# Kernel optimization log

Measured on AMD Instinct MI355X. Metric: run time of the kernel, lower is better.

The kernel has to match this reference:

```python
import jax, jax.numpy as jnp
import numpy as np

DIM = 1024
HEADS = 16
DIM_HEAD = 64
INNER = HEADS * DIM_HEAD  # 1024
P = INNER  # num_param_tokens
B, N = 4, 2048
LN_EPS = 1e-5
NORM_EPS = 1e-12


def _pattention(x, key_tok, val_tok):
    # x: [..., dim_in]; key_tok: [P, dim_in]; val_tok: [P, dim_out]
    scale = key_tok.shape[1] ** (-0.5)
    sim = jnp.einsum('bnd,pd->bnp', x, key_tok) * scale
    # F.normalize(p=2, dim=-1) with eps=1e-12
    nrm = jnp.maximum(jnp.linalg.norm(sim, axis=-1, keepdims=True), NORM_EPS)
    attn = jax.nn.gelu(sim / nrm, approximate=False)  # torch F.gelu default = exact erf
    return jnp.einsum('bnp,pe->bne', attn, val_tok)


def setup_inputs() -> dict:
    key = jax.random.key(0)
    ks = jax.random.split(key, 11)
    d = {
        'x': jax.random.normal(ks[0], (B, N, DIM), dtype=jnp.float32),
        'ln_gamma': jnp.ones((DIM,), dtype=jnp.float32),
        'ln_beta': jnp.zeros((DIM,), dtype=jnp.float32),
        'q_key': jax.random.normal(ks[1], (P, DIM), dtype=jnp.float32),
        'q_val': jax.random.normal(ks[2], (P, INNER), dtype=jnp.float32),
        'k_key': jax.random.normal(ks[3], (P, DIM), dtype=jnp.float32),
        'k_val': jax.random.normal(ks[4], (P, INNER), dtype=jnp.float32),
        'v_key': jax.random.normal(ks[5], (P, DIM), dtype=jnp.float32),
        'v_val': jax.random.normal(ks[6], (P, INNER), dtype=jnp.float32),
        'o_key': jax.random.normal(ks[7], (P, INNER), dtype=jnp.float32),
        'o_val': jax.random.normal(ks[8], (P, DIM), dtype=jnp.float32),
    }
    return d


def reference(x, ln_gamma, ln_beta, q_key, q_val, k_key, k_val, v_key, v_val, o_key, o_val):
    # LayerNorm (torch default: elementwise affine, eps=1e-5)
    mu = jnp.mean(x, axis=-1, keepdims=True)
    var = jnp.mean(jnp.square(x - mu), axis=-1, keepdims=True)
    x_norm = (x - mu) / jnp.sqrt(var + LN_EPS) * ln_gamma + ln_beta

    q = _pattention(x_norm, q_key, q_val)  # [B, N, INNER]
    k = _pattention(x_norm, k_key, k_val)
    v = _pattention(x_norm, v_key, v_val)

    # b n (h d) -> b h n d
    def split_heads(t):
        return t.reshape(B, N, HEADS, DIM_HEAD).transpose(0, 2, 1, 3)

    q, k, v = split_heads(q), split_heads(k), split_heads(v)
    scale = DIM_HEAD ** (-0.5)
    dots = jnp.einsum('bhnd,bhmd->bhnm', q, k) * scale  # [B, H, N, N]
    attn = jax.nn.softmax(dots, axis=-1)  # dropout p=0 -> identity
    out = jnp.einsum('bhnm,bhmd->bhnd', attn, v)
    out = out.transpose(0, 2, 1, 3).reshape(B, N, INNER)  # b h n d -> b n (h d)
    return _pattention(out, o_key, o_val)
```

## Files before the change

kernel.cpp:

```cpp
#include <hip/hip_runtime.h>
#include <hip/hip_bf16.h>
#include <stdint.h>

#define DIMSZ 1024
#define BN_TOT 8192
#define NSEQ 2048
#define NHEADS 16
#define DHEAD 64

typedef __attribute__((ext_vector_type(8))) __bf16 bf16x8;
typedef __attribute__((ext_vector_type(4))) float f32x4;

__device__ __forceinline__ float bf2f(ushort u) {
  return __uint_as_float(((uint32_t)u) << 16);
}
__device__ __forceinline__ ushort f2bf(float f) {
  uint32_t u = __float_as_uint(f);
  u += 0x7FFFu + ((u >> 16) & 1u);
  return (ushort)(u >> 16);
}
__device__ __forceinline__ uint32_t cvt_pk_bf16(float lo, float hi) {
  uint32_t r;
  asm("v_cvt_pk_bf16_f32 %0, %1, %2" : "=v"(r) : "v"(lo), "v"(hi));
  return r;
}
__device__ __forceinline__ void gl_lds16(const ushort* g, ushort* l) {
  __builtin_amdgcn_global_load_lds(
      (const __attribute__((address_space(1))) void*)g,
      (__attribute__((address_space(3))) void*)l, 16, 0, 0);
}

__global__ __launch_bounds__(256) void layernorm_k(
    const float* __restrict__ x, const float* __restrict__ gamma,
    const float* __restrict__ beta, ushort* __restrict__ xn) {
  const int row = blockIdx.x;
  const int tid = threadIdx.x;
  const float* xr = x + (size_t)row * DIMSZ;
  float4 v = *(const float4*)(xr + tid * 4);
  float s = v.x + v.y + v.z + v.w;
  float ss = v.x * v.x + v.y * v.y + v.z * v.z + v.w * v.w;
#pragma unroll
  for (int o = 1; o < 64; o <<= 1) { s += __shfl_xor(s, o); ss += __shfl_xor(ss, o); }
  __shared__ float red[2][4];
  const int wid = tid >> 6;
  if ((tid & 63) == 0) { red[0][wid] = s; red[1][wid] = ss; }
  __syncthreads();
  s = red[0][0] + red[0][1] + red[0][2] + red[0][3];
  ss = red[1][0] + red[1][1] + red[1][2] + red[1][3];
  const float mu = s * (1.0f / DIMSZ);
  const float var = ss * (1.0f / DIMSZ) - mu * mu;
  const float rstd = rsqrtf(var + 1e-5f);
  float4 g = *(const float4*)(gamma + tid * 4);
  float4 bb = *(const float4*)(beta + tid * 4);
  ushort4 o4;
  o4.x = f2bf((v.x - mu) * rstd * g.x + bb.x);
  o4.y = f2bf((v.y - mu) * rstd * g.y + bb.y);
  o4.z = f2bf((v.z - mu) * rstd * g.z + bb.z);
  o4.w = f2bf((v.w - mu) * rstd * g.w + bb.w);
  *(ushort4*)(xn + (size_t)row * DIMSZ + tid * 4) = o4;
}

__global__ __launch_bounds__(256) void normgelu_k(
    const float* __restrict__ sim, ushort* __restrict__ out) {
  const int row = blockIdx.x;
  const int tid = threadIdx.x;
  const float* sr = sim + (size_t)row * DIMSZ;
  float4 v = *(const float4*)(sr + tid * 4);
  float ss = v.x * v.x + v.y * v.y + v.z * v.z + v.w * v.w;
#pragma unroll
  for (int o = 1; o < 64; o <<= 1) ss += __shfl_xor(ss, o);
  __shared__ float red[4];
  if ((tid & 63) == 0) red[tid >> 6] = ss;
  __syncthreads();
  ss = red[0] + red[1] + red[2] + red[3];
  const float inv = 1.0f / fmaxf(sqrtf(ss), 1e-12f);
  ushort4 o4;
  float x0;
  x0 = v.x * inv; o4.x = f2bf(0.5f * x0 * (1.0f + erff(x0 * 0.70710678118654752f)));
  x0 = v.y * inv; o4.y = f2bf(0.5f * x0 * (1.0f + erff(x0 * 0.70710678118654752f)));
  x0 = v.z * inv; o4.z = f2bf(0.5f * x0 * (1.0f + erff(x0 * 0.70710678118654752f)));
  x0 = v.w * inv; o4.w = f2bf(0.5f * x0 * (1.0f + erff(x0 * 0.70710678118654752f)));
  *(ushort4*)(out + (size_t)row * DIMSZ + tid * 4) = o4;
}

__global__ void cvt_k(const float* __restrict__ in, ushort* __restrict__ out, int n) {
  int i = (blockIdx.x * 256 + threadIdx.x) * 4;
  if (i < n) {
    float4 v = *(const float4*)(in + i);
    ushort4 o;
    o.x = f2bf(v.x); o.y = f2bf(v.y); o.z = f2bf(v.z); o.w = f2bf(v.w);
    *(ushort4*)(out + i) = o;
  }
}

__global__ __launch_bounds__(256) void transpose_cvt_k(
    const float* __restrict__ in, ushort* __restrict__ out) {
  __shared__ float t[32][33];
  const int tx = threadIdx.x & 31;
  const int ty = threadIdx.x >> 5;
  const int bx = blockIdx.x * 32;
  const int by = blockIdx.y * 32;
#pragma unroll
  for (int i = 0; i < 32; i += 8)
    t[ty + i][tx] = in[(size_t)(by + ty + i) * DIMSZ + bx + tx];
  __syncthreads();
#pragma unroll
  for (int i = 0; i < 32; i += 8)
    out[(size_t)(bx + ty + i) * DIMSZ + by + tx] = f2bf(t[tx][ty + i]);
}

__global__ __launch_bounds__(256) void transpose_v_k(
    const ushort* __restrict__ vb, ushort* __restrict__ vt) {
  __shared__ ushort t[32][33];
  const int bh = blockIdx.x;
  const int nt = blockIdx.y;
  const int dt = blockIdx.z;
  const int b = bh >> 4, h = bh & 15;
  const int tx = threadIdx.x & 31;
  const int ty = threadIdx.x >> 5;
  const size_t inbase = ((size_t)b * NSEQ + nt * 32) * DIMSZ + h * DHEAD + dt * 32;
#pragma unroll
  for (int i = 0; i < 32; i += 8)
    t[ty + i][tx] = vb[inbase + (size_t)(ty + i) * DIMSZ + tx];
  __syncthreads();
  const size_t outbase = ((size_t)bh * DHEAD + dt * 32) * NSEQ + nt * 32;
#pragma unroll
  for (int i = 0; i < 32; i += 8)
    vt[outbase + (size_t)(ty + i) * NSEQ + tx] = t[tx][ty + i];
}

template <int OUT_BF16>
__global__ __launch_bounds__(256) void gemm_nt_k(
    const ushort* __restrict__ A, const ushort* __restrict__ B,
    void* __restrict__ Cout, int M, int N, int K) {
  __shared__ ushort As[3][128 * 32];
  __shared__ ushort Bs[3][128 * 32];
  const int tid = threadIdx.x;
  const int lane = tid & 63;
  const int wid = tid >> 6;
  const int i0 = blockIdx.x * 128;
  const int n0 = blockIdx.y * 128;
  const int wr = (wid >> 1) * 64;
  const int wc = (wid & 1) * 64;
  f32x4 acc[4][4];
#pragma unroll
  for (int m = 0; m < 4; ++m)
#pragma unroll
    for (int n = 0; n < 4; ++n) acc[m][n] = (f32x4){0.f, 0.f, 0.f, 0.f};
  const int fr = lane & 15;
  const int g = lane >> 4;
  const int kg = (g ^ ((fr >> 1) & 3)) * 8;
  const int srow = wid * 32 + (lane >> 2);
  const int skc = ((lane & 3) ^ ((lane >> 3) & 3)) * 8;
  const ushort* Ag = A + (size_t)(i0 + srow) * K + skc;
  const ushort* Bg = B + (size_t)(n0 + srow) * K + skc;
  const int wb = wid * 1024;

#define STAGE_TILE(tt, bb)                                      \
  do {                                                          \
    gl_lds16(Ag + (tt) * 32, &As[bb][wb]);                      \
    gl_lds16(Ag + (size_t)16 * K + (tt) * 32, &As[bb][wb + 512]); \
    gl_lds16(Bg + (tt) * 32, &Bs[bb][wb]);                      \
    gl_lds16(Bg + (size_t)16 * K + (tt) * 32, &Bs[bb][wb + 512]); \
  } while (0)

  const int nt = K >> 5;
  STAGE_TILE(0, 0);
  STAGE_TILE(1, 1);
  asm volatile("s_waitcnt vmcnt(4)" ::: "memory");
  __builtin_amdgcn_s_barrier();

  int cur = 0;
  for (int t = 0; t < nt; ++t) {
    if (t + 2 < nt) {
      const int nb = (cur >= 1) ? cur - 1 : cur + 2;
      STAGE_TILE(t + 2, nb);
    }
    bf16x8 af[4], bfr[4];
#pragma unroll
    for (int m = 0; m < 4; ++m)
      af[m] = *(const bf16x8*)&As[cur][(wr + m * 16 + fr) * 32 + kg];
#pragma unroll
    for (int n = 0; n < 4; ++n)
      bfr[n] = *(const bf16x8*)&Bs[cur][(wc + n * 16 + fr) * 32 + kg];
#pragma unroll
    for (int m = 0; m < 4; ++m)
#pragma unroll
      for (int n = 0; n < 4; ++n)
        acc[m][n] = __builtin_amdgcn_mfma_f32_16x16x32_bf16(af[m], bfr[n], acc[m][n], 0, 0, 0);
    if (t + 2 < nt)
      asm volatile("s_waitcnt vmcnt(4)" ::: "memory");
    else
      asm volatile("s_waitcnt vmcnt(0)" ::: "memory");
    __builtin_amdgcn_s_barrier();
    cur = (cur == 2) ? 0 : cur + 1;
  }
#undef STAGE_TILE

  const int rq = lane >> 4;
#pragma unroll
  for (int m = 0; m < 4; ++m) {
#pragma unroll
    for (int n = 0; n < 4; ++n) {
#pragma unroll
      for (int rr = 0; rr < 4; ++rr) {
        const int row = i0 + wr + m * 16 + rq * 4 + rr;
        const int col = n0 + wc + n * 16 + fr;
        if (OUT_BF16)
          ((ushort*)Cout)[(size_t)row * N + col] = f2bf(acc[m][n][rr]);
        else
          ((float*)Cout)[(size_t)row * N + col] = acc[m][n][rr];
      }
    }
  }
}

__global__ __launch_bounds__(256) void flash_mfma_k(
    const ushort* __restrict__ Qm, const ushort* __restrict__ Km,
    const ushort* __restrict__ Vt, ushort* __restrict__ Om) {
  __shared__ ushort Ks[64 * 72];
  __shared__ ushort Vs[65 * 72];
  __shared__ ushort Ps[4][32 * 72];
  const int tid = threadIdx.x;
  const int lane = tid & 63;
  const int wid = tid >> 6;
  const int bh = blockIdx.x;
  const int qb = blockIdx.y;
  const int bidx = bh >> 4;
  const int h = bh & 15;
  const size_t rowbase = (size_t)bidx * NSEQ;
  const int colbase = h * DHEAD;
  const int fr = lane & 15;
  const int g = lane >> 4;
  const int kg = g * 8;
  const int q0 = qb * 128 + wid * 32;

  if (tid < 64) Vs[64 * 72 + tid] = 0x3F80;

  bf16x8 qf[2][2];
#pragma unroll
  for (int m = 0; m < 2; ++m)
#pragma unroll
    for (int ks = 0; ks < 2; ++ks)
      qf[m][ks] = *(const bf16x8*)(Qm + (rowbase + q0 + m * 16 + fr) * (size_t)DIMSZ +
                                   colbase + ks * 32 + kg);

  f32x4 oaccT[2][4];
  f32x4 lacc[2];
#pragma unroll
  for (int m = 0; m < 2; ++m) {
#pragma unroll
    for (int n = 0; n < 4; ++n) oaccT[m][n] = (f32x4){0.f, 0.f, 0.f, 0.f};
    lacc[m] = (f32x4){0.f, 0.f, 0.f, 0.f};
  }
  float m2[2] = {-1e30f, -1e30f};
  const float c1 = 0.125f * 1.44269504088896340736f;

  const ushort* Kg = Km + rowbase * DIMSZ + colbase;
  const ushort* Vg = Vt + (size_t)bh * DHEAD * NSEQ;
  const int sr = tid >> 3;
  const int c8 = (tid & 7) * 8;

  uint4 k0 = *(const uint4*)(Kg + (size_t)sr * DIMSZ + c8);
  uint4 k1 = *(const uint4*)(Kg + (size_t)(sr + 32) * DIMSZ + c8);
  uint4 v0 = *(const uint4*)(Vg + (size_t)sr * NSEQ + c8);
  uint4 v1 = *(const uint4*)(Vg + (size_t)(sr + 32) * NSEQ + c8);

  for (int kt = 0; kt < NSEQ / 64; ++kt) {
    __syncthreads();
    *(uint4*)&Ks[sr * 72 + c8] = k0;
    *(uint4*)&Ks[(sr + 32) * 72 + c8] = k1;
    *(uint4*)&Vs[sr * 72 + c8] = v0;
    *(uint4*)&Vs[(sr + 32) * 72 + c8] = v1;
    __syncthreads();
    if (kt + 1 < NSEQ / 64) {
      k0 = *(const uint4*)(Kg + (size_t)((kt + 1) * 64 + sr) * DIMSZ + c8);
      k1 = *(const uint4*)(Kg + (size_t)((kt + 1) * 64 + sr + 32) * DIMSZ + c8);
      v0 = *(const uint4*)(Vg + (size_t)sr * NSEQ + (kt + 1) * 64 + c8);
      v1 = *(const uint4*)(Vg + (size_t)(sr + 32) * NSEQ + (kt + 1) * 64 + c8);
    }

    f32x4 s[2][4];
#pragma unroll
    for (int m = 0; m < 2; ++m)
#pragma unroll
      for (int n = 0; n < 4; ++n) s[m][n] = (f32x4){0.f, 0.f, 0.f, 0.f};
    __builtin_amdgcn_s_setprio(1);
#pragma unroll
    for (int ks = 0; ks < 2; ++ks) {
      bf16x8 ak[4];
#pragma unroll
      for (int n = 0; n < 4; ++n)
        ak[n] = *(const bf16x8*)&Ks[(n * 16 + fr) * 72 + ks * 32 + kg];
#pragma unroll
      for (int m = 0; m < 2; ++m)
#pragma unroll
        for (int n = 0; n < 4; ++n)
          s[m][n] = __builtin_amdgcn_mfma_f32_16x16x32_bf16(ak[n], qf[m][ks], s[m][n], 0, 0, 0);
    }
    __builtin_amdgcn_s_setprio(0);

#pragma unroll
    for (int m = 0; m < 2; ++m) {
      const float a0 = fmaxf(fmaxf(s[m][0][0], s[m][0][1]), s[m][0][2]);
      const float a1 = fmaxf(fmaxf(s[m][0][3], s[m][1][0]), s[m][1][1]);
      const float a2 = fmaxf(fmaxf(s[m][1][2], s[m][1][3]), s[m][2][0]);
      const float a3 = fmaxf(fmaxf(s[m][2][1], s[m][2][2]), s[m][2][3]);
      const float a4 = fmaxf(fmaxf(s[m][3][0], s[m][3][1]), s[m][3][2]);
      const float b0 = fmaxf(fmaxf(a0, a1), a2);
      const float b1 = fmaxf(fmaxf(a3, a4), s[m][3][3]);
      float tm = fmaxf(b0, b1);
      tm = fmaxf(tm, __shfl_xor(tm, 16));
      tm = fmaxf(tm, __shfl_xor(tm, 32));
      const float tm2 = tm * c1;
      if (!__all(tm2 <= m2[m] + 8.0f)) {
        const float mn2 = fmaxf(m2[m], tm2);
        const float al = exp2f(m2[m] - mn2);
        m2[m] = mn2;
        lacc[m] *= al;
#pragma unroll
        for (int n = 0; n < 4; ++n) oaccT[m][n] *= al;
      }
      const float mref = m2[m];
#pragma unroll
      for (int n = 0; n < 4; ++n)
#pragma unroll
        for (int rr = 0; rr < 4; ++rr)
          s[m][n][rr] = exp2f(fmaf(s[m][n][rr], c1, -mref));
    }

    ushort* pw = &Ps[wid][0];
#pragma unroll
    for (int m = 0; m < 2; ++m)
#pragma unroll
      for (int n = 0; n < 4; ++n) {
        uint2 w;
        w.x = cvt_pk_bf16(s[m][n][0], s[m][n][1]);
        w.y = cvt_pk_bf16(s[m][n][2], s[m][n][3]);
        *(uint2*)&pw[(m * 16 + fr) * 72 + n * 16 + g * 4] = w;
      }

    __builtin_amdgcn_s_setprio(1);
#pragma unroll
    for (int ks = 0; ks < 2; ++ks) {
      bf16x8 av[4], pb[2];
      const bf16x8 av1 = *(const bf16x8*)&Vs[64 * 72 + ks * 32 + kg];
#pragma unroll
      for (int nd = 0; nd < 4; ++nd)
        av[nd] = *(const bf16x8*)&Vs[(nd * 16 + fr) * 72 + ks * 32 + kg];
#pragma unroll
      for (int m = 0; m < 2; ++m)
        pb[m] = *(const bf16x8*)&Ps[wid][(m * 16 + fr) * 72 + ks * 32 + kg];
#pragma unroll
      for (int m = 0; m < 2; ++m) {
#pragma unroll
        for (int nd = 0; nd < 4; ++nd)
          oaccT[m][nd] = __builtin_amdgcn_mfma_f32_16x16x32_bf16(av[nd], pb[m], oaccT[m][nd], 0, 0, 0);
        lacc[m] = __builtin_amdgcn_mfma_f32_16x16x32_bf16(av1, pb[m], lacc[m], 0, 0, 0);
      }
    }
    __builtin_amdgcn_s_setprio(0);
  }

#pragma unroll
  for (int m = 0; m < 2; ++m) {
    const float invl = 1.0f / lacc[m][0];
    const size_t row = rowbase + q0 + m * 16 + fr;
#pragma unroll
    for (int nd = 0; nd < 4; ++nd) {
      uint2 w;
      w.x = cvt_pk_bf16(oaccT[m][nd][0] * invl, oaccT[m][nd][1] * invl);
      w.y = cvt_pk_bf16(oaccT[m][nd][2] * invl, oaccT[m][nd][3] * invl);
      *(uint2*)(Om + row * DIMSZ + colbase + nd * 16 + g * 4) = w;
    }
  }
}

extern "C" void kernel_launch(void* const* d_in, const int* in_sizes, int n_in,
                              void* d_out, int out_size, void* d_ws, size_t ws_size,
                              hipStream_t stream) {
  (void)in_sizes; (void)n_in; (void)out_size; (void)ws_size;
  const float* x     = (const float*)d_in[0];
  const float* ln_g  = (const float*)d_in[1];
  const float* ln_b  = (const float*)d_in[2];
  const float* q_key = (const float*)d_in[3];
  const float* q_val = (const float*)d_in[4];
  const float* k_key = (const float*)d_in[5];
  const float* k_val = (const float*)d_in[6];
  const float* v_key = (const float*)d_in[7];
  const float* v_val = (const float*)d_in[8];
  const float* o_key = (const float*)d_in[9];
  const float* o_val = (const float*)d_in[10];
  float* out = (float*)d_out;

  char* ws = (char*)d_ws;
  const size_t MB = 1024 * 1024;
  ushort* xn    = (ushort*)(ws + 0 * MB);
  ushort* wkey  = (ushort*)(ws + 16 * MB);
  ushort* wvalT = (ushort*)(ws + 24 * MB);
  ushort* gelu  = (ushort*)(ws + 32 * MB);
  ushort* qb    = (ushort*)(ws + 48 * MB);
  ushort* kb    = (ushort*)(ws + 64 * MB);
  ushort* vb    = (ushort*)(ws + 80 * MB);
  ushort* aout  = (ushort*)(ws + 96 * MB);
  ushort* vt    = gelu;
  float* sim = (float*)d_out;

  const int NW = DIMSZ * DIMSZ;

  layernorm_k<<<BN_TOT, 256, 0, stream>>>(x, ln_g, ln_b, xn);
  cvt_k<<<1024, 256, 0, stream>>>(q_key, wkey + 0 * (size_t)NW, NW);
  cvt_k<<<1024, 256, 0, stream>>>(k_key, wkey + 1 * (size_t)NW, NW);
  cvt_k<<<1024, 256, 0, stream>>>(v_key, wkey + 2 * (size_t)NW, NW);
  cvt_k<<<1024, 256, 0, stream>>>(o_key, wkey + 3 * (size_t)NW, NW);
  dim3 tg(32, 32);
  transpose_cvt_k<<<tg, 256, 0, stream>>>(q_val, wvalT + 0 * (size_t)NW);
  transpose_cvt_k<<<tg, 256, 0, stream>>>(k_val, wvalT + 1 * (size_t)NW);
  transpose_cvt_k<<<tg, 256, 0, stream>>>(v_val, wvalT + 2 * (size_t)NW);
  transpose_cvt_k<<<tg, 256, 0, stream>>>(o_val, wvalT + 3 * (size_t)NW);

  dim3 gg(BN_TOT / 128, DIMSZ / 128);
  ushort* outs[3] = {qb, kb, vb};
  for (int t = 0; t < 3; ++t) {
    gemm_nt_k<0><<<gg, 256, 0, stream>>>(xn, wkey + t * (size_t)NW, sim, BN_TOT, DIMSZ, DIMSZ);
    normgelu_k<<<BN_TOT, 256, 0, stream>>>(sim, gelu);
    gemm_nt_k<1><<<gg, 256, 0, stream>>>(gelu, wvalT + t * (size_t)NW, outs[t], BN_TOT, DIMSZ, DIMSZ);
  }
  transpose_v_k<<<dim3(64, 64, 2), 256, 0, stream>>>(vb, vt);
  flash_mfma_k<<<dim3(64, 16), 256, 0, stream>>>(qb, kb, vt, aout);
  gemm_nt_k<0><<<gg, 256, 0, stream>>>(aout, wkey + 3 * (size_t)NW, sim, BN_TOT, DIMSZ, DIMSZ);
  normgelu_k<<<BN_TOT, 256, 0, stream>>>(sim, gelu);
  gemm_nt_k<0><<<gg, 256, 0, stream>>>(gelu, wvalT + 3 * (size_t)NW, (void*)out, BN_TOT, DIMSZ, DIMSZ);
}
```

Baseline: 440.4 us.

## Batch QKV pattention GEMMs, fuse row sum-of-squares into GEMM epilogue, store sim as bf16

The three Q/K/V key and value GEMMs now run as single launches with a z grid dimension, and the weight conversions are batched into one launch each. The key GEMM's epilogue accumulates per-row sums of squares via shuffles and atomicAdd. It writes sim as bf16 instead of fp32, so the normalize+GELU pass becomes a single in-place elementwise bf16 pass with no block reduction. This cuts launch count, fp32 traffic and the reduction cost. In exchange it adds atomics, a memset, and extra rounding because sim is stored in bf16 before normalization.

```diff
diff --git a/kernel.cpp b/kernel.cpp
--- a/kernel.cpp
+++ b/kernel.cpp
@@ -60,42 +60,41 @@
   *(ushort4*)(xn + (size_t)row * DIMSZ + tid * 4) = o4;
 }
 
-__global__ __launch_bounds__(256) void normgelu_k(
-    const float* __restrict__ sim, ushort* __restrict__ out) {
-  const int row = blockIdx.x;
-  const int tid = threadIdx.x;
-  const float* sr = sim + (size_t)row * DIMSZ;
-  float4 v = *(const float4*)(sr + tid * 4);
-  float ss = v.x * v.x + v.y * v.y + v.z * v.z + v.w * v.w;
-#pragma unroll
-  for (int o = 1; o < 64; o <<= 1) ss += __shfl_xor(ss, o);
-  __shared__ float red[4];
-  if ((tid & 63) == 0) red[tid >> 6] = ss;
-  __syncthreads();
-  ss = red[0] + red[1] + red[2] + red[3];
-  const float inv = 1.0f / fmaxf(sqrtf(ss), 1e-12f);
+__global__ __launch_bounds__(256) void normgelu_bf_k(
+    ushort* __restrict__ buf, const float* __restrict__ ssq) {
+  const size_t row = (size_t)blockIdx.y * BN_TOT + blockIdx.x;
+  ushort* p = buf + row * DIMSZ + threadIdx.x * 4;
+  const float inv = 1.0f / fmaxf(sqrtf(ssq[row]), 1e-12f);
+  ushort4 v = *(const ushort4*)p;
   ushort4 o4;
   float x0;
-  x0 = v.x * inv; o4.x = f2bf(0.5f * x0 * (1.0f + erff(x0 * 0.70710678118654752f)));
-  x0 = v.y * inv; o4.y = f2bf(0.5f * x0 * (1.0f + erff(x0 * 0.70710678118654752f)));
-  x0 = v.z * inv; o4.z = f2bf(0.5f * x0 * (1.0f + erff(x0 * 0.70710678118654752f)));
-  x0 = v.w * inv; o4.w = f2bf(0.5f * x0 * (1.0f + erff(x0 * 0.70710678118654752f)));
-  *(ushort4*)(out + (size_t)row * DIMSZ + tid * 4) = o4;
-}
-
-__global__ void cvt_k(const float* __restrict__ in, ushort* __restrict__ out, int n) {
-  int i = (blockIdx.x * 256 + threadIdx.x) * 4;
-  if (i < n) {
-    float4 v = *(const float4*)(in + i);
-    ushort4 o;
-    o.x = f2bf(v.x); o.y = f2bf(v.y); o.z = f2bf(v.z); o.w = f2bf(v.w);
-    *(ushort4*)(out + i) = o;
-  }
-}
-
-__global__ __launch_bounds__(256) void transpose_cvt_k(
-    const float* __restrict__ in, ushort* __restrict__ out) {
+  x0 = bf2f(v.x) * inv; o4.x = f2bf(0.5f * x0 * (1.0f + erff(x0 * 0.70710678118654752f)));
+  x0 = bf2f(v.y) * inv; o4.y = f2bf(0.5f * x0 * (1.0f + erff(x0 * 0.70710678118654752f)));
+  x0 = bf2f(v.z) * inv; o4.z = f2bf(0.5f * x0 * (1.0f + erff(x0 * 0.70710678118654752f)));
+  x0 = bf2f(v.w) * inv; o4.w = f2bf(0.5f * x0 * (1.0f + erff(x0 * 0.70710678118654752f)));
+  *(ushort4*)p = o4;
+}
+
+__global__ void cvt4_k(const float* __restrict__ s0, const float* __restrict__ s1,
+                       const float* __restrict__ s2, const float* __restrict__ s3,
+                       ushort* __restrict__ out) {
+  const int z = blockIdx.z;
+  const float* in = (z == 0) ? s0 : (z == 1) ? s1 : (z == 2) ? s2 : s3;
+  const int i = (blockIdx.x * 256 + threadIdx.x) * 4;
+  float4 v = *(const float4*)(in + i);
+  ushort4 o;
+  o.x = f2bf(v.x); o.y = f2bf(v.y); o.z = f2bf(v.z); o.w = f2bf(v.w);
+  *(ushort4*)(out + (size_t)z * DIMSZ * DIMSZ + i) = o;
+}
+
+__global__ __launch_bounds__(256) void transpose_cvt4_k(
+    const float* __restrict__ s0, const float* __restrict__ s1,
+    const float* __restrict__ s2, const float* __restrict__ s3,
+    ushort* __restrict__ out) {
   __shared__ float t[32][33];
+  const int z = blockIdx.z;
+  const float* in = (z == 0) ? s0 : (z == 1) ? s1 : (z == 2) ? s2 : s3;
+  ushort* dst = out + (size_t)z * DIMSZ * DIMSZ;
   const int tx = threadIdx.x & 31;
   const int ty = threadIdx.x >> 5;
   const int bx = blockIdx.x * 32;
@@ -106,7 +105,7 @@
   __syncthreads();
 #pragma unroll
   for (int i = 0; i < 32; i += 8)
-    out[(size_t)(bx + ty + i) * DIMSZ + by + tx] = f2bf(t[tx][ty + i]);
+    dst[(size_t)(bx + ty + i) * DIMSZ + by + tx] = f2bf(t[tx][ty + i]);
 }
 
 __global__ __launch_bounds__(256) void transpose_v_k(
@@ -129,12 +128,18 @@
     vt[outbase + (size_t)(ty + i) * NSEQ + tx] = t[tx][ty + i];
 }
 
-template <int OUT_BF16>
+template <int OUT_BF16, int WRITE_SSQ, int A_PER_Z>
 __global__ __launch_bounds__(256) void gemm_nt_k(
     const ushort* __restrict__ A, const ushort* __restrict__ B,
-    void* __restrict__ Cout, int M, int N, int K) {
+    void* __restrict__ C0, void* __restrict__ C1, void* __restrict__ C2,
+    float* __restrict__ ssq, int M, int N, int K) {
   __shared__ ushort As[3][128 * 32];
   __shared__ ushort Bs[3][128 * 32];
+  const int z = blockIdx.z;
+  const ushort* Az = A + (A_PER_Z ? (size_t)z * M * K : 0);
+  const ushort* Bz = B + (size_t)z * N * K;
+  void* Cout = (z == 0) ? C0 : (z == 1) ? C1 : C2;
+  float* sz = WRITE_SSQ ? (ssq + (size_t)z * M) : nullptr;
   const int tid = threadIdx.x;
   const int lane = tid & 63;
   const int wid = tid >> 6;
@@ -152,8 +157,8 @@
   const int kg = (g ^ ((fr >> 1) & 3)) * 8;
   const int srow = wid * 32 + (lane >> 2);
   const int skc = ((lane & 3) ^ ((lane >> 3) & 3)) * 8;
-  const ushort* Ag = A + (size_t)(i0 + srow) * K + skc;
-  const ushort* Bg = B + (size_t)(n0 + srow) * K + skc;
+  const ushort* Ag = Az + (size_t)(i0 + srow) * K + skc;
+  const ushort* Bg = Bz + (size_t)(n0 + srow) * K + skc;
   const int wb = wid * 1024;
 
 #define STAGE_TILE(tt, bb)                                      \
@@ -210,6 +215,19 @@
           ((ushort*)Cout)[(size_t)row * N + col] = f2bf(acc[m][n][rr]);
         else
           ((float*)Cout)[(size_t)row * N + col] = acc[m][n][rr];
+      }
+    }
+  }
+  if (WRITE_SSQ) {
+#pragma unroll
+    for (int m = 0; m < 4; ++m) {
+#pragma unroll
+      for (int rr = 0; rr < 4; ++rr) {
+        float s2 = acc[m][0][rr] * acc[m][0][rr] + acc[m][1][rr] * acc[m][1][rr] +
+                   acc[m][2][rr] * acc[m][2][rr] + acc[m][3][rr] * acc[m][3][rr];
+#pragma unroll
+        for (int o = 1; o < 16; o <<= 1) s2 += __shfl_xor(s2, o);
+        if (fr == 0) atomicAdd(&sz[i0 + wr + m * 16 + rq * 4 + rr], s2);
       }
     }
   }
@@ -398,37 +416,36 @@
   ushort* xn    = (ushort*)(ws + 0 * MB);
   ushort* wkey  = (ushort*)(ws + 16 * MB);
   ushort* wvalT = (ushort*)(ws + 24 * MB);
-  ushort* gelu  = (ushort*)(ws + 32 * MB);
-  ushort* qb    = (ushort*)(ws + 48 * MB);
-  ushort* kb    = (ushort*)(ws + 64 * MB);
-  ushort* vb    = (ushort*)(ws + 80 * MB);
-  ushort* aout  = (ushort*)(ws + 96 * MB);
-  ushort* vt    = gelu;
-  float* sim = (float*)d_out;
+  ushort* bufA  = (ushort*)(ws + 32 * MB);
+  ushort* bufB  = (ushort*)(ws + 48 * MB);
+  ushort* bufC  = (ushort*)(ws + 64 * MB);
+  ushort* bufD  = (ushort*)(ws + 80 * MB);
+  ushort* bufE  = (ushort*)(ws + 96 * MB);
+  ushort* vscr  = (ushort*)d_out;
+  float*  ssqb  = (float*)((char*)d_out + 24 * MB);
 
   const int NW = DIMSZ * DIMSZ;
 
+  hipMemsetAsync(ssqb, 0, 4 * BN_TOT * sizeof(float), stream);
   layernorm_k<<<BN_TOT, 256, 0, stream>>>(x, ln_g, ln_b, xn);
-  cvt_k<<<1024, 256, 0, stream>>>(q_key, wkey + 0 * (size_t)NW, NW);
-  cvt_k<<<1024, 256, 0, stream>>>(k_key, wkey + 1 * (size_t)NW, NW);
-  cvt_k<<<1024, 256, 0, stream>>>(v_key, wkey + 2 * (size_t)NW, NW);
-  cvt_k<<<1024, 256, 0, stream>>>(o_key, wkey + 3 * (size_t)NW, NW);
-  dim3 tg(32, 32);
-  transpose_cvt_k<<<tg, 256, 0, stream>>>(q_val, wvalT + 0 * (size_t)NW);
-  transpose_cvt_k<<<tg, 256, 0, stream>>>(k_val, wvalT + 1 * (size_t)NW);
-  transpose_cvt_k<<<tg, 256, 0, stream>>>(v_val, wvalT + 2 * (size_t)NW);
-  transpose_cvt_k<<<tg, 256, 0, stream>>>(o_val, wvalT + 3 * (size_t)NW);
-
-  dim3 gg(BN_TOT / 128, DIMSZ / 128);
-  ushort* outs[3] = {qb, kb, vb};
-  for (int t = 0; t < 3; ++t) {
-    gemm_nt_k<0><<<gg, 256, 0, stream>>>(xn, wkey + t * (size_t)NW, sim, BN_TOT, DIMSZ, DIMSZ);
-    normgelu_k<<<BN_TOT, 256, 0, stream>>>(sim, gelu);
-    gemm_nt_k<1><<<gg, 256, 0, stream>>>(gelu, wvalT + t * (size_t)NW, outs[t], BN_TOT, DIMSZ, DIMSZ);
-  }
-  transpose_v_k<<<dim3(64, 64, 2), 256, 0, stream>>>(vb, vt);
-  flash_mfma_k<<<dim3(64, 16), 256, 0, stream>>>(qb, kb, vt, aout);
-  gemm_nt_k<0><<<gg, 256, 0, stream>>>(aout, wkey + 3 * (size_t)NW, sim, BN_TOT, DIMSZ, DIMSZ);
-  normgelu_k<<<BN_TOT, 256, 0, stream>>>(sim, gelu);
-  gemm_nt_k<0><<<gg, 256, 0, stream>>>(gelu, wvalT + 3 * (size_t)NW, (void*)out, BN_TOT, DIMSZ, DIMSZ);
-}
+  cvt4_k<<<dim3(1024, 1, 4), 256, 0, stream>>>(q_key, k_key, v_key, o_key, wkey);
+  transpose_cvt4_k<<<dim3(32, 32, 4), 256, 0, stream>>>(q_val, k_val, v_val, o_val, wvalT);
+
+  dim3 gg3(BN_TOT / 128, DIMSZ / 128, 3);
+  dim3 gg1(BN_TOT / 128, DIMSZ / 128, 1);
+  gemm_nt_k<1, 1, 0><<<gg3, 256, 0, stream>>>(
+      xn, wkey, bufB, bufC, bufD, ssqb, BN_TOT, DIMSZ, DIMSZ);
+  normgelu_bf_k<<<dim3(BN_TOT, 3), 256, 0, stream>>>(bufB, ssqb);
+  gemm_nt_k<1, 0, 1><<<gg3, 256, 0, stream>>>(
+      bufB, wvalT, bufA, bufE, vscr, nullptr, BN_TOT, DIMSZ, DIMSZ);
+
+  transpose_v_k<<<dim3(64, 64, 2), 256, 0, stream>>>(vscr, bufD);
+  flash_mfma_k<<<dim3(64, 16), 256, 0, stream>>>(bufA, bufE, bufD, bufB);
+
+  gemm_nt_k<1, 1, 0><<<gg1, 256, 0, stream>>>(
+      bufB, wkey + 3 * (size_t)NW, bufC, bufC, bufC, ssqb + 3 * BN_TOT,
+      BN_TOT, DIMSZ, DIMSZ);
+  normgelu_bf_k<<<dim3(BN_TOT, 1), 256, 0, stream>>>(bufC, ssqb + 3 * BN_TOT);
+  gemm_nt_k<0, 0, 0><<<gg1, 256, 0, stream>>>(
+      bufC, wvalT + 3 * (size_t)NW, out, out, out, nullptr, BN_TOT, DIMSZ, DIMSZ);
+}
```

After: 397.5 us. 9.7% less time.
